# Performance work log

Hardware: AMD Instinct MI355X
Metric: run time of the kernel (lower is better)

Reference implementation:

```python
import jax, jax.numpy as jnp
import numpy as np
from jax import lax

# ---- fixed RPN/FPN configuration (torchvision defaults) ----
LEVEL_HW = [(200, 200), (100, 100), (50, 50), (25, 25), (13, 13)]
STRIDES = [4, 8, 16, 32, 64]
SIZES = [32.0, 64.0, 128.0, 256.0, 512.0]
RATIOS = [0.5, 1.0, 2.0]
A = len(RATIOS)
NUM_PER_LEVEL = [A * h * w for h, w in LEVEL_HW]
T = sum(NUM_PER_LEVEL)
N_IMG = 8
IMG_H = IMG_W = 800.0
PRE_NMS = 1000   # per level
POST_NMS = 1000
NMS_TH = 0.7
MIN_SIZE = 1e-3
BBOX_CLIP = float(np.log(1000.0 / 16.0))


def _make_anchors():
    all_a = []
    for (h, w), s, size in zip(LEVEL_HW, STRIDES, SIZES):
        base = []
        for r in RATIOS:
            bw = size / np.sqrt(r)
            bh = size * np.sqrt(r)
            base.append([-bw / 2, -bh / 2, bw / 2, bh / 2])
        base = np.asarray(base, np.float32)                      # [A,4]
        ys = (np.arange(h, dtype=np.float32) + 0.5) * s
        xs = (np.arange(w, dtype=np.float32) + 0.5) * s
        cy, cx = np.meshgrid(ys, xs, indexing='ij')
        shifts = np.stack([cx, cy, cx, cy], -1).reshape(-1, 1, 4)  # [H*W,1,4]
        all_a.append((shifts + base[None]).reshape(-1, 4))         # [H*W*A,4]
    return np.concatenate(all_a, 0)                                # [T,4]


def setup_inputs() -> dict:
    key = jax.random.key(0)
    k1, k2 = jax.random.split(key)
    objectness = jax.random.normal(k1, (N_IMG, T), jnp.float32)
    deltas = jax.random.normal(k2, (N_IMG, T, 4), jnp.float32) * 0.2
    anchors = jnp.asarray(_make_anchors())
    return {"objectness": objectness, "deltas": deltas, "anchors": anchors}


def _decode(deltas, anchors):
    # BoxCoder.decode with weights (1,1,1,1)
    w = anchors[:, 2] - anchors[:, 0]
    h = anchors[:, 3] - anchors[:, 1]
    cx = anchors[:, 0] + 0.5 * w
    cy = anchors[:, 1] + 0.5 * h
    dx, dy, dw, dh = deltas[..., 0], deltas[..., 1], deltas[..., 2], deltas[..., 3]
    dw = jnp.minimum(dw, BBOX_CLIP)
    dh = jnp.minimum(dh, BBOX_CLIP)
    pcx = dx * w + cx
    pcy = dy * h + cy
    pw = jnp.exp(dw) * w
    ph = jnp.exp(dh) * h
    return jnp.stack([pcx - 0.5 * pw, pcy - 0.5 * ph,
                      pcx + 0.5 * pw, pcy + 0.5 * ph], axis=-1)  # [N,T,4]


def _pairwise_iou(b):
    area = (b[:, 2] - b[:, 0]) * (b[:, 3] - b[:, 1])
    lt = jnp.maximum(b[:, None, :2], b[None, :, :2])
    rb = jnp.minimum(b[:, None, 2:], b[None, :, 2:])
    wh = jnp.clip(rb - lt, 0.0)
    inter = wh[..., 0] * wh[..., 1]
    return inter / (area[:, None] + area[None, :] - inter)


def _per_image(args):
    boxes, logit, lvl = args          # [K,4], [K], [K]
    # clip to image
    x1 = jnp.clip(boxes[:, 0], 0.0, IMG_W)
    y1 = jnp.clip(boxes[:, 1], 0.0, IMG_H)
    x2 = jnp.clip(boxes[:, 2], 0.0, IMG_W)
    y2 = jnp.clip(boxes[:, 3], 0.0, IMG_H)
    boxes_c = jnp.stack([x1, y1, x2, y2], -1)
    # small-box filter -> mask via -inf score
    valid = (x2 - x1 >= MIN_SIZE) & (y2 - y1 >= MIN_SIZE)
    scores = jax.nn.sigmoid(logit)
    s = jnp.where(valid, scores, -jnp.inf)
    # batched NMS: offset boxes per level so cross-level IoU == 0
    max_c = boxes_c.max()
    off = lvl.astype(boxes_c.dtype) * (max_c + 1.0)
    bn = boxes_c + off[:, None]
    order = jnp.argsort(-s)
    b = bn[order]
    sv = s[order]
    so = scores[order]
    bo = boxes_c[order]
    K = b.shape[0]
    iou = _pairwise_iou(b)
    idx = jnp.arange(K)

    def body(i, supp):
        alive = jnp.logical_not(supp[i])
        sup_i = alive & (iou[i] > NMS_TH) & (idx > i)
        return supp | sup_i

    supp = lax.fori_loop(0, K, body, jnp.zeros((K,), bool))
    keep = jnp.logical_not(supp) & jnp.isfinite(sv)
    sel_s = jnp.where(keep, sv, -jnp.inf)
    vals, sel = lax.top_k(sel_s, POST_NMS)      # post-nms top-n (sorted desc)
    vmask = jnp.isfinite(vals)
    out_boxes = jnp.where(vmask[:, None], bo[sel], 0.0)
    out_scores = jnp.where(vmask, so[sel], 0.0)
    return jnp.concatenate([out_boxes, out_scores[:, None]], -1)  # [P,5]


def reference(objectness, deltas, anchors):
    proposals = _decode(deltas, anchors)            # [N,T,4]
    # per-level top-k of objectness (get_top_n_idx)
    idxs = []
    offset = 0
    for n in NUM_PER_LEVEL:
        ob = lax.slice_in_dim(objectness, offset, offset + n, axis=1)
        k = min(PRE_NMS, n)
        _, top = lax.top_k(ob, k)
        idxs.append(top + offset)
        offset += n
    top_idx = jnp.concatenate(idxs, axis=1)         # [N,K]
    levels_full = jnp.concatenate(
        [jnp.full((n,), i, jnp.int32) for i, n in enumerate(NUM_PER_LEVEL)])
    logit_g = jnp.take_along_axis(objectness, top_idx, axis=1)          # [N,K]
    props_g = jnp.take_along_axis(proposals, top_idx[..., None], axis=1)  # [N,K,4]
    lvl_g = levels_full[top_idx]                                        # [N,K]
    out = lax.map(_per_image, (props_g, logit_g, lvl_g))                # [N,P,5]
    return out
```

## Files before the change

kernel.cpp:

```cpp
#include <hip/hip_runtime.h>
#include <math.h>

#define NIMG 8
#define TT   159882
#define KTOT 4507
#define POST 1000
#define NSUB 32

__constant__ int c_n[5]   = {120000,30000,7500,1875,507};
__constant__ int c_off[5] = {0,120000,150000,157500,159375};
__constant__ int c_k[5]   = {1000,1000,1000,1000,507};
__constant__ int c_pos[5] = {0,1000,2000,3000,4000};

__device__ __forceinline__ unsigned fkey(float f){
  unsigned u=__float_as_uint(f);
  return (u&0x80000000u)? ~u : (u|0x80000000u);
}

__global__ __launch_bounds__(256) void k_zero(unsigned* __restrict__ ghist,
                                              int* __restrict__ grank,
                                              unsigned* __restrict__ gmaxu){
  int i=blockIdx.x*256+threadIdx.x;
  if(i<40*2048) ghist[i]=0u;
  int j=i-40*2048;
  if(j>=0 && j<NIMG*KTOT) grank[j]=0;
  int j2=j-NIMG*KTOT;
  if(j2>=0 && j2<NIMG) gmaxu[j2]=0u;
}

template<int RND>
__global__ __launch_bounds__(256) void k_hist(const float* __restrict__ obj,
    const unsigned* __restrict__ gpref, unsigned* __restrict__ ghist){
  constexpr int sh=(RND==0)?21:10;
  constexpr unsigned msk=2047u;
  const int il=blockIdx.x, sub=blockIdx.y;
  const int img=il/5, lvl=il%5;
  const int n=c_n[lvl], k=c_k[lvl];
  if(k>=n) return;
  const int chunk=(n+NSUB-1)/NSUB;
  const int start=sub*chunk, end=min(start+chunk,n);
  if(start>=end) return;
  const float* o=obj+(size_t)img*TT+c_off[lvl];
  __shared__ unsigned hist[2048];
  const unsigned prefix=(RND==0)?0u:gpref[il];
  for(int i=threadIdx.x;i<2048;i+=256) hist[i]=0u;
  __syncthreads();
  for(int i=start+threadIdx.x;i<end;i+=256){
    unsigned key=fkey(o[i]);
    if(RND==0){
      atomicAdd(&hist[(key>>sh)&msk],1u);
    } else {
      if((key&0xFFE00000u)==prefix) atomicAdd(&hist[(key>>sh)&msk],1u);
    }
  }
  __syncthreads();
  for(int b=threadIdx.x;b<2048;b+=256){
    unsigned v=hist[b];
    if(v) atomicAdd(&ghist[il*2048+b],v);
  }
}

template<int RND>
__global__ __launch_bounds__(256) void k_scan(unsigned* __restrict__ ghist,
    unsigned* __restrict__ gpref, int* __restrict__ gkrem,
    int* __restrict__ gcnt){
  constexpr int sh=(RND==0)?21:10;
  constexpr int C=8;
  const int il=blockIdx.x, lvl=il%5;
  const int n=c_n[lvl], k=c_k[lvl];
  const int t=threadIdx.x;
  __shared__ unsigned tot[256];
  if(k>=n){
    if(RND==1 && t==0){ gpref[il]=0u; gkrem[il]=0; gcnt[il*2]=0; gcnt[il*2+1]=0; }
    return;
  }
  const int kr=(RND==0)?k:gkrem[il];
  unsigned v[C];
#pragma unroll
  for(int i=0;i<C;i++) v[i]=ghist[il*2048+t*C+i];
#pragma unroll
  for(int i=C-2;i>=0;i--) v[i]+=v[i+1];
  tot[t]=v[0];
  __syncthreads();
#pragma unroll
  for(int d=1;d<256;d<<=1){
    unsigned add=(t+d<256)?tot[t+d]:0u;
    __syncthreads();
    tot[t]+=add;
    __syncthreads();
  }
  unsigned tail=(t<255)?tot[t+1]:0u;
#pragma unroll
  for(int i=0;i<C;i++){
    unsigned suf=v[i]+tail;
    unsigned sufn=((i<C-1)?v[i+1]:0u)+tail;
    if(suf>=(unsigned)kr && sufn<(unsigned)kr){
      unsigned prevPref=(RND==0)?0u:gpref[il];
      gpref[il]=prevPref|((unsigned)(t*C+i)<<sh);
      gkrem[il]=kr-(int)sufn;
    }
  }
  for(int b=t;b<2048;b+=256) ghist[il*2048+b]=0u;
  if(RND==1 && t==0){ gcnt[il*2]=0; gcnt[il*2+1]=0; }
}

__global__ __launch_bounds__(256) void k_sel(const float* __restrict__ obj,
    const unsigned* __restrict__ gpref, const int* __restrict__ gkrem,
    int* __restrict__ gcnt, int* __restrict__ sel, int* __restrict__ eqbuf){
  const int il=blockIdx.x, sub=blockIdx.y;
  const int img=il/5, lvl=il%5;
  const int n=c_n[lvl], k=c_k[lvl];
  const int chunk=(n+NSUB-1)/NSUB;
  const int start=sub*chunk, end=min(start+chunk,n);
  if(start>=end) return;
  int* s=sel+img*KTOT+c_pos[lvl];
  if(k>=n){
    for(int i=start+threadIdx.x;i<end;i+=256) s[i]=i;
    return;
  }
  __shared__ int s_gt[1024];
  __shared__ int s_eq[2048];
  __shared__ int cnt_gt, cnt_eq, base_gt, base_eq;
  if(threadIdx.x==0){ cnt_gt=0; cnt_eq=0; }
  __syncthreads();
  const float* o=obj+(size_t)img*TT+c_off[lvl];
  const unsigned t=gpref[il];
  const int krem=gkrem[il];
  for(int i=start+threadIdx.x;i<end;i+=256){
    unsigned mk=fkey(o[i])&0xFFFFFC00u;
    if(mk>t){ int p=atomicAdd(&cnt_gt,1); s_gt[p]=i; }
    else if(mk==t && krem>0){ int p=atomicAdd(&cnt_eq,1); if(p<2048) s_eq[p]=i; }
  }
  __syncthreads();
  const int cg=cnt_gt, ce=min(cnt_eq,2048);
  if(threadIdx.x==0) base_gt=(cg>0)? atomicAdd(&gcnt[il*2],cg) : 0;
  if(threadIdx.x==1) base_eq=(ce>0)? atomicAdd(&gcnt[il*2+1],ce) : 0;
  __syncthreads();
  for(int i=threadIdx.x;i<cg;i+=256) s[base_gt+i]=s_gt[i];
  for(int i=threadIdx.x;i<ce;i+=256){
    int p=base_eq+i;
    if(p<2048) eqbuf[il*2048+p]=s_eq[i];
  }
}

__global__ __launch_bounds__(256) void k_sortd(const float* __restrict__ obj,
    const int* __restrict__ gkrem, const int* __restrict__ gcnt,
    const int* __restrict__ sel, int* __restrict__ sel2,
    const int* __restrict__ eqbuf){
  const int il=blockIdx.x, chunk=blockIdx.y;
  const int img=il/5, lvl=il%5;
  const int n=c_n[lvl], k=c_k[lvl];
  if(chunk*256>=k) return;
  const float* o=obj+(size_t)img*TT+c_off[lvl];
  const int* s=sel+img*KTOT+c_pos[lvl];
  int* s2=sel2+img*KTOT+c_pos[lvl];
  __shared__ unsigned long long skey[1024];
  __shared__ unsigned long long eqk[2048];
  int cgt, krem;
  if(k<n){ cgt=gcnt[il*2]; krem=gkrem[il]; } else { cgt=k; krem=0; }
  const int ceq = (krem>0)? min(gcnt[il*2+1],2048) : 0;
  for(int i=threadIdx.x;i<cgt;i+=256){
    int idx=s[i];
    skey[i]=((unsigned long long)fkey(o[idx])<<32)|(unsigned)(~(unsigned)idx);
  }
  for(int i=threadIdx.x;i<ceq;i+=256){
    int idx=eqbuf[il*2048+i];
    eqk[i]=((unsigned long long)fkey(o[idx])<<32)|(unsigned)(~(unsigned)idx);
  }
  __syncthreads();
  if(krem>0 && threadIdx.x==0){
    for(int r2=0;r2<krem;r2++){
      unsigned long long best=0ull; int bi=0;
      for(int j=0;j<ceq;j++){ unsigned long long kk=eqk[j]; if(kk>best){best=kk;bi=j;} }
      skey[cgt+r2]=best; eqk[bi]=0ull;
    }
  }
  __syncthreads();
  const int i=chunk*256+threadIdx.x;
  if(i>=k) return;
  const unsigned long long mk=skey[i];
  int rank=0, j=0;
  const int k8=k&~7;
  for(;j<k8;j+=8){
    unsigned long long a0=skey[j  ],a1=skey[j+1],a2=skey[j+2],a3=skey[j+3];
    unsigned long long a4=skey[j+4],a5=skey[j+5],a6=skey[j+6],a7=skey[j+7];
    rank+=((a0>mk)?1:0)+((a1>mk)?1:0)+((a2>mk)?1:0)+((a3>mk)?1:0)
         +((a4>mk)?1:0)+((a5>mk)?1:0)+((a6>mk)?1:0)+((a7>mk)?1:0);
  }
  for(;j<k;j++) rank+=(skey[j]>mk)?1:0;
  int idx=(int)(~(unsigned)(mk&0xFFFFFFFFu));
  s2[rank]=idx+c_off[lvl];
}

__global__ __launch_bounds__(256) void k_decode(const float* __restrict__ obj,
    const float* __restrict__ del, const float* __restrict__ anc,
    const int* __restrict__ sel, float* __restrict__ pbox, float* __restrict__ pscore,
    int* __restrict__ plvl, unsigned long long* __restrict__ gkey,
    unsigned* __restrict__ gmaxu){
  const int img=blockIdx.x/18, chunk=blockIdx.x%18;
  const int pos=chunk*256+threadIdx.x;
  __shared__ float smax[256];
  const float BCLIP=(float)4.135166556742356;
  float lm=0.f;
  if(pos<KTOT){
    int lvl = pos<1000?0:pos<2000?1:pos<3000?2:pos<4000?3:4;
    int tdx = sel[img*KTOT+pos];
    float logit = obj[(size_t)img*TT+tdx];
    const float* a=anc+4*(size_t)tdx;
    const float* d=del+((size_t)img*TT+tdx)*4;
    float w=a[2]-a[0], h=a[3]-a[1];
    float cx=a[0]+0.5f*w, cy=a[1]+0.5f*h;
    float dw=fminf(d[2],BCLIP), dh=fminf(d[3],BCLIP);
    float pcx=d[0]*w+cx, pcy=d[1]*h+cy;
    float pw=expf(dw)*w, ph=expf(dh)*h;
    float x1=pcx-0.5f*pw, y1=pcy-0.5f*ph;
    float x2=pcx+0.5f*pw, y2=pcy+0.5f*ph;
    x1=fminf(fmaxf(x1,0.f),800.f); y1=fminf(fmaxf(y1,0.f),800.f);
    x2=fminf(fmaxf(x2,0.f),800.f); y2=fminf(fmaxf(y2,0.f),800.f);
    int valid=(x2-x1>=1e-3f)&&(y2-y1>=1e-3f);
    float sc=1.f/(1.f+expf(-logit));
    float sv=valid? sc : -INFINITY;
    gkey[img*KTOT+pos]=((unsigned long long)fkey(sv)<<32)|(unsigned)(KTOT-1-pos);
    float* pb=pbox+((size_t)img*KTOT+pos)*4;
    pb[0]=x1; pb[1]=y1; pb[2]=x2; pb[3]=y2;
    pscore[img*KTOT+pos]=sc;
    plvl[img*KTOT+pos]=lvl|(valid?0:256);
    lm=fmaxf(fmaxf(x1,y1),fmaxf(x2,y2));
  }
  smax[threadIdx.x]=lm; __syncthreads();
  for(int st=128;st>0;st>>=1){
    if(threadIdx.x<st) smax[threadIdx.x]=fmaxf(smax[threadIdx.x],smax[threadIdx.x+st]);
    __syncthreads();
  }
  if(threadIdx.x==0) atomicMax(&gmaxu[img], __float_as_uint(smax[0]));
}

__global__ __launch_bounds__(256) void k_rankp(const unsigned long long* __restrict__ gkey,
    int* __restrict__ grank){
  const int img=blockIdx.x, ic=blockIdx.y, jc=blockIdx.z;
  __shared__ unsigned long long sk[256];
  const int jbase=jc*256;
  const int jend=min(256, KTOT-jbase);
  const int i=ic*256+threadIdx.x;
  if(threadIdx.x<jend) sk[threadIdx.x]=gkey[img*KTOT+jbase+threadIdx.x];
  __syncthreads();
  if(i>=KTOT) return;
  const unsigned long long mk=gkey[img*KTOT+i];
  int r=0;
  #pragma unroll 4
  for(int j=0;j<jend;j++) r+=(sk[j]>mk)?1:0;
  if(r) atomicAdd(&grank[img*KTOT+i], r);
}

__global__ __launch_bounds__(256) void k_scatter(const int* __restrict__ grank,
    const float4* __restrict__ pbox, const float* __restrict__ pscore,
    const int* __restrict__ plvl,
    float4* __restrict__ sbox, float* __restrict__ sscore,
    int* __restrict__ slvl, int* __restrict__ ssupp){
  const int img=blockIdx.x/18, chunk=blockIdx.x%18;
  const int pos=chunk*256+threadIdx.x;
  if(pos>=KTOT) return;
  const int rank=grank[img*KTOT+pos];
  sbox[(size_t)img*KTOT+rank]=pbox[(size_t)img*KTOT+pos];
  sscore[img*KTOT+rank]=pscore[img*KTOT+pos];
  int lv=plvl[img*KTOT+pos];
  slvl[img*KTOT+rank]=lv&0xFF;
  ssupp[img*KTOT+rank]=(lv>>8)&1;
}

__global__ __launch_bounds__(256) void k_list(const float* __restrict__ sbox,
    const int* __restrict__ slvl, const int* __restrict__ ssupp,
    const unsigned* __restrict__ gmaxu,
    int* __restrict__ lists, int* __restrict__ mcnt,
    float4* __restrict__ nbox, float* __restrict__ narea){
  const int img=blockIdx.x/5, lvl=blockIdx.x%5;
  const int tid=threadIdx.x;
  __shared__ unsigned char s_ok[KTOT];
  __shared__ int s_list[1024];
  __shared__ int s_m;
  for(int i=tid;i<KTOT;i+=256)
    s_ok[i]=(slvl[img*KTOT+i]==lvl && ssupp[img*KTOT+i]==0)?1:0;
  __syncthreads();
  if(tid<64){
    int base=0;
    for(int t=0;t<KTOT;t+=64){
      int r=t+tid;
      bool pred=(r<KTOT) && s_ok[r];
      unsigned long long b=__ballot(pred);
      int pre=__popcll(b & ((1ull<<tid)-1ull));
      if(pred) s_list[base+pre]=r;
      base+=__popcll(b);
    }
    if(tid==0){ s_m=base; mcnt[blockIdx.x]=base; }
  }
  __syncthreads();
  const int m=s_m;
  const float off=(float)lvl*(__uint_as_float(gmaxu[img])+1.0f);
  const float4* sb4=(const float4*)sbox;
  for(int i=tid;i<m;i+=256){
    int r=s_list[i];
    lists[blockIdx.x*1024+i]=r;
    float4 bx=sb4[(size_t)img*KTOT+r];
    float a0=bx.x+off, a1=bx.y+off, a2=bx.z+off, a3=bx.w+off;
    nbox[blockIdx.x*1024+i]=make_float4(a0,a1,a2,a3);
    narea[blockIdx.x*1024+i]=(a2-a0)*(a3-a1);
  }
}

__global__ __launch_bounds__(256) void k_mask(const float4* __restrict__ nbox,
    const float* __restrict__ narea, const int* __restrict__ mcnt,
    unsigned long long* __restrict__ mask){
  const int il=blockIdx.x;
  const int rc=blockIdx.y>>4, w=blockIdx.y&15;
  const int m=mcnt[il];
  const int r0=rc*256;
  if(r0>=m) return;
  const int i=r0+threadIdx.x;
  const int wlast=(m+63)>>6;
  __shared__ float4 sb[64];
  __shared__ float  sa[64];
  unsigned long long bits=0ull;
  const bool block_active = (w>=rc*4) && (w<wlast);
  if(block_active){
    const int jend=min(64, m-w*64);
    if(threadIdx.x<64 && threadIdx.x<jend){
      sb[threadIdx.x]=nbox[il*1024+w*64+threadIdx.x];
      sa[threadIdx.x]=narea[il*1024+w*64+threadIdx.x];
    }
    __syncthreads();
    const int wi=i>>6;
    if(i<m && w>=wi){
      const float4 bi=nbox[il*1024+i];
      const float  ai=narea[il*1024+i];
      for(int jj=0;jj<jend;++jj){
        const float4 bj=sb[jj];
        float ltx=fmaxf(bi.x,bj.x), lty=fmaxf(bi.y,bj.y);
        float rbx=fminf(bi.z,bj.z), rby=fminf(bi.w,bj.w);
        float wx=fmaxf(rbx-ltx,0.f), wy=fmaxf(rby-lty,0.f);
        float inter=wx*wy;
        float iou=inter/((ai+sa[jj])-inter);
        bits |= (iou>0.7f)? (1ull<<jj) : 0ull;
      }
      if(w==wi){ int b=i&63; bits &= ~((2ull<<b)-1ull); }
    }
  }
  if(i<m) mask[((size_t)il*1024+i)*16+w]=bits;
}

__global__ __launch_bounds__(256) void k_reduce(const unsigned long long* __restrict__ mask,
    const int* __restrict__ mcnt, const int* __restrict__ lists,
    int* __restrict__ ssupp){
  const int il=blockIdx.x, img=il/5;
  const int m=mcnt[il];
  const int m_pad=(m+15)&~15;
  __shared__ unsigned long long smask[1024*16];
  {
    const float4* g4=(const float4*)(mask + (size_t)il*1024*16);
    float4* l4=(float4*)smask;
    const int tot4=(m*8+2047)&~2047;
    for(int i=threadIdx.x;i<tot4;i+=2048){
      float4 r0=g4[i      ], r1=g4[i+ 256], r2=g4[i+ 512], r3=g4[i+ 768];
      float4 r4=g4[i+1024], r5=g4[i+1280], r6=g4[i+1536], r7=g4[i+1792];
      l4[i      ]=r0; l4[i+ 256]=r1; l4[i+ 512]=r2; l4[i+ 768]=r3;
      l4[i+1024]=r4; l4[i+1280]=r5; l4[i+1536]=r6; l4[i+1792]=r7;
    }
  }
  __syncthreads();
  if(threadIdx.x<(m_pad-m)*16) smask[(unsigned)m*16+threadIdx.x]=0ull;
  __syncthreads();
  if(threadIdx.x>=64) return;
  const int lane=threadIdx.x;
  const int seg=lane&15;
  unsigned long long remv=0ull;
  unsigned long long c0,c1,c2,c3,c4,c5,c6,c7,c8,c9,c10,c11,c12,c13,c14,c15;
  unsigned long long n0,n1,n2,n3,n4,n5,n6,n7,n8,n9,n10,n11,n12,n13,n14,n15;
#define LD(r,b) smask[(unsigned)((b)+(r))*16+seg]
  c0 =LD(0,0);  c1 =LD(1,0);  c2 =LD(2,0);  c3 =LD(3,0);
  c4 =LD(4,0);  c5 =LD(5,0);  c6 =LD(6,0);  c7 =LD(7,0);
  c8 =LD(8,0);  c9 =LD(9,0);  c10=LD(10,0); c11=LD(11,0);
  c12=LD(12,0); c13=LD(13,0); c14=LD(14,0); c15=LD(15,0);
  for(int g=0;;++g){
    const int nb=(g+1)*16;
    n0 =LD(0,nb);  n1 =LD(1,nb);  n2 =LD(2,nb);  n3 =LD(3,nb);
    n4 =LD(4,nb);  n5 =LD(5,nb);  n6 =LD(6,nb);  n7 =LD(7,nb);
    n8 =LD(8,nb);  n9 =LD(9,nb);  n10=LD(10,nb); n11=LD(11,nb);
    n12=LD(12,nb); n13=LD(13,nb); n14=LD(14,nb); n15=LD(15,nb);
    const int base=g*16;
    const int w=base>>6;
    const int bb=base&63;
    unsigned t8=(unsigned)(remv>>bb);
    unsigned am=0u;
#define DEC(r,cr) { unsigned alive=1u^((t8>>(r))&1u); am|=alive<<(r); \
                    if(alive) t8|=(unsigned)((cr)>>bb); }
    DEC(0,c0)  DEC(1,c1)  DEC(2,c2)  DEC(3,c3)
    DEC(4,c4)  DEC(5,c5)  DEC(6,c6)  DEC(7,c7)
    DEC(8,c8)  DEC(9,c9)  DEC(10,c10) DEC(11,c11)
    DEC(12,c12) DEC(13,c13) DEC(14,c14) DEC(15,c15)
#undef DEC
    unsigned am_w=__builtin_amdgcn_readlane(am, w);
#define APP(r,cr) { unsigned long long mk64=0ull-(unsigned long long)((am_w>>(r))&1u); \
                    remv|=(cr)&mk64; }
    APP(0,c0)  APP(1,c1)  APP(2,c2)  APP(3,c3)
    APP(4,c4)  APP(5,c5)  APP(6,c6)  APP(7,c7)
    APP(8,c8)  APP(9,c9)  APP(10,c10) APP(11,c11)
    APP(12,c12) APP(13,c13) APP(14,c14) APP(15,c15)
#undef APP
    if(nb>=m) break;
    c0 =n0;  c1 =n1;  c2 =n2;  c3 =n3;  c4 =n4;  c5 =n5;  c6 =n6;  c7 =n7;
    c8 =n8;  c9 =n9;  c10=n10; c11=n11; c12=n12; c13=n13; c14=n14; c15=n15;
  }
#undef LD
  const int* list = lists + il*1024;
  for(int t=0;t<m;t+=64){
    int i=t+lane;
    unsigned long long word=__shfl(remv, (i<m? i:0)>>6);
    if(i<m && ((word>>(i&63))&1ull)) ssupp[img*KTOT+list[i]]=1;
  }
}

__global__ __launch_bounds__(256) void k_out(const float* __restrict__ sbox,
    const float* __restrict__ sscore, const int* __restrict__ ssupp,
    float* __restrict__ out){
  const int img=blockIdx.x;
  const int tid=threadIdx.x;
  __shared__ unsigned char s_ok[KTOT];
  __shared__ unsigned short list[POST];
  __shared__ int s_c;
  for(int i=tid;i<KTOT;i+=256) s_ok[i]=(ssupp[img*KTOT+i]==0)?1:0;
  __syncthreads();
  if(tid<64){
    int base=0;
    for(int t=0;t<KTOT && base<POST;t+=64){
      int r=t+tid;
      bool pred=(r<KTOT) && s_ok[r];
      unsigned long long b=__ballot(pred);
      int pre=__popcll(b & ((1ull<<tid)-1ull));
      if(pred && base+pre<POST) list[base+pre]=(unsigned short)r;
      base+=__popcll(b);
    }
    if(tid==0) s_c=min(base,POST);
  }
  __syncthreads();
  const int c=s_c;
  for(int o=tid;o<POST;o+=256){
    float* row=out+((size_t)img*POST+o)*5;
    if(o<c){
      int r=list[o];
      const float* b=sbox+((size_t)img*KTOT+r)*4;
      row[0]=b[0]; row[1]=b[1]; row[2]=b[2]; row[3]=b[3];
      row[4]=sscore[img*KTOT+r];
    } else {
      row[0]=0.f; row[1]=0.f; row[2]=0.f; row[3]=0.f; row[4]=0.f;
    }
  }
}

extern "C" void kernel_launch(void* const* d_in, const int* in_sizes, int n_in,
                              void* d_out, int out_size, void* d_ws, size_t ws_size,
                              hipStream_t stream){
  const float* obj=(const float*)d_in[0];
  const float* del=(const float*)d_in[1];
  const float* anc=(const float*)d_in[2];
  float* out=(float*)d_out;

  char* w=(char*)d_ws;
  size_t off=0;
  auto alloc=[&](size_t bytes)->void*{
    void* p=w+off; off+=(bytes+255)&~(size_t)255; return p;
  };
  int*  sel    =(int*)  alloc(sizeof(int)*NIMG*KTOT);
  int*  sel2   =(int*)  alloc(sizeof(int)*NIMG*KTOT);
  float* pbox  =(float*)alloc(sizeof(float)*NIMG*KTOT*4);
  float* pscore=(float*)alloc(sizeof(float)*NIMG*KTOT);
  int*  plvl   =(int*)  alloc(sizeof(int)*NIMG*KTOT);
  unsigned long long* gkey=(unsigned long long*)alloc(sizeof(unsigned long long)*NIMG*KTOT);
  float* sbox  =(float*)alloc(sizeof(float)*NIMG*KTOT*4);
  float* sscore=(float*)alloc(sizeof(float)*NIMG*KTOT);
  int*  slvl   =(int*)  alloc(sizeof(int)*NIMG*KTOT);
  int*  ssupp  =(int*)  alloc(sizeof(int)*NIMG*KTOT);
  unsigned* gmaxu=(unsigned*)alloc(sizeof(unsigned)*NIMG);
  int*  eqbuf  =(int*)  alloc(sizeof(int)*40*2048);
  int*  lists  =(int*)  alloc(sizeof(int)*40*1024);
  int*  mcnt   =(int*)  alloc(sizeof(int)*40);
  float4* nbox =(float4*)alloc(sizeof(float4)*40*1024);
  float* narea =(float*)alloc(sizeof(float)*40*1024);
  unsigned long long* mask=(unsigned long long*)alloc(sizeof(unsigned long long)*40*1024*16);
  unsigned* ghist=(unsigned*)alloc(sizeof(unsigned)*40*2048);
  unsigned* gpref=(unsigned*)alloc(sizeof(unsigned)*40);
  int*  gkrem  =(int*)  alloc(sizeof(int)*40);
  int*  gcnt   =(int*)  alloc(sizeof(int)*80);
  int*  grank  =(int*)  alloc(sizeof(int)*NIMG*KTOT);

  hipLaunchKernelGGL(k_zero,    dim3((40*2048+NIMG*KTOT+NIMG+255)/256), dim3(256), 0, stream,
                     ghist, grank, gmaxu);
  hipLaunchKernelGGL(k_hist<0>, dim3(40,NSUB), dim3(256), 0, stream, obj, gpref, ghist);
  hipLaunchKernelGGL(k_scan<0>, dim3(40), dim3(256), 0, stream, ghist, gpref, gkrem, gcnt);
  hipLaunchKernelGGL(k_hist<1>, dim3(40,NSUB), dim3(256), 0, stream, obj, gpref, ghist);
  hipLaunchKernelGGL(k_scan<1>, dim3(40), dim3(256), 0, stream, ghist, gpref, gkrem, gcnt);
  hipLaunchKernelGGL(k_sel,    dim3(40,NSUB), dim3(256), 0, stream, obj, gpref, gkrem,
                     gcnt, sel, eqbuf);
  hipLaunchKernelGGL(k_sortd,  dim3(40,4), dim3(256), 0, stream, obj, gkrem, gcnt,
                     sel, sel2, eqbuf);
  hipLaunchKernelGGL(k_decode, dim3(NIMG*18), dim3(256), 0, stream, obj, del, anc, sel2,
                     pbox, pscore, plvl, gkey, gmaxu);
  hipLaunchKernelGGL(k_rankp,  dim3(NIMG,18,18), dim3(256), 0, stream, gkey, grank);
  hipLaunchKernelGGL(k_scatter,dim3(NIMG*18), dim3(256), 0, stream, grank,
                     (const float4*)pbox, pscore, plvl,
                     (float4*)sbox, sscore, slvl, ssupp);
  hipLaunchKernelGGL(k_list,   dim3(40), dim3(256), 0, stream, sbox, slvl, ssupp, gmaxu,
                     lists, mcnt, nbox, narea);
  hipLaunchKernelGGL(k_mask,   dim3(40,64), dim3(256), 0, stream, nbox, narea, mcnt, mask);
  hipLaunchKernelGGL(k_reduce, dim3(40), dim3(256), 0, stream, mask, mcnt, lists, ssupp);
  hipLaunchKernelGGL(k_out,    dim3(NIMG), dim3(256), 0, stream, sbox, sscore, ssupp, out);
}
```

Baseline: 152.1 us.

## Replace two-pass radix top-k select with single pass plus parallel tie ranking

Result: slower. 392.1 us (+157.8%).

```diff
diff --git a/kernel.cpp b/kernel.cpp
--- a/kernel.cpp
+++ b/kernel.cpp
@@ -18,21 +18,15 @@
 }
 
 __global__ __launch_bounds__(256) void k_zero(unsigned* __restrict__ ghist,
-                                              int* __restrict__ grank,
-                                              unsigned* __restrict__ gmaxu){
+                                              int* __restrict__ grank){
   int i=blockIdx.x*256+threadIdx.x;
   if(i<40*2048) ghist[i]=0u;
   int j=i-40*2048;
   if(j>=0 && j<NIMG*KTOT) grank[j]=0;
-  int j2=j-NIMG*KTOT;
-  if(j2>=0 && j2<NIMG) gmaxu[j2]=0u;
-}
-
-template<int RND>
+}
+
 __global__ __launch_bounds__(256) void k_hist(const float* __restrict__ obj,
-    const unsigned* __restrict__ gpref, unsigned* __restrict__ ghist){
-  constexpr int sh=(RND==0)?21:10;
-  constexpr unsigned msk=2047u;
+    unsigned* __restrict__ ghist){
   const int il=blockIdx.x, sub=blockIdx.y;
   const int img=il/5, lvl=il%5;
   const int n=c_n[lvl], k=c_k[lvl];
@@ -42,16 +36,11 @@
   if(start>=end) return;
   const float* o=obj+(size_t)img*TT+c_off[lvl];
   __shared__ unsigned hist[2048];
-  const unsigned prefix=(RND==0)?0u:gpref[il];
   for(int i=threadIdx.x;i<2048;i+=256) hist[i]=0u;
   __syncthreads();
   for(int i=start+threadIdx.x;i<end;i+=256){
     unsigned key=fkey(o[i]);
-    if(RND==0){
-      atomicAdd(&hist[(key>>sh)&msk],1u);
-    } else {
-      if((key&0xFFE00000u)==prefix) atomicAdd(&hist[(key>>sh)&msk],1u);
-    }
+    atomicAdd(&hist[key>>21],1u);
   }
   __syncthreads();
   for(int b=threadIdx.x;b<2048;b+=256){
@@ -60,21 +49,21 @@
   }
 }
 
-template<int RND>
 __global__ __launch_bounds__(256) void k_scan(unsigned* __restrict__ ghist,
     unsigned* __restrict__ gpref, int* __restrict__ gkrem,
-    int* __restrict__ gcnt){
-  constexpr int sh=(RND==0)?21:10;
+    int* __restrict__ gcnt, unsigned* __restrict__ gmaxu){
   constexpr int C=8;
   const int il=blockIdx.x, lvl=il%5;
   const int n=c_n[lvl], k=c_k[lvl];
   const int t=threadIdx.x;
   __shared__ unsigned tot[256];
+  if(t==0 && il<NIMG) gmaxu[il]=0u;
+  if(t==0){ gcnt[il*2]=0; gcnt[il*2+1]=0; }
   if(k>=n){
-    if(RND==1 && t==0){ gpref[il]=0u; gkrem[il]=0; gcnt[il*2]=0; gcnt[il*2+1]=0; }
+    if(t==0){ gpref[il]=0u; gkrem[il]=0; }
     return;
   }
-  const int kr=(RND==0)?k:gkrem[il];
+  const int kr=k;
   unsigned v[C];
 #pragma unroll
   for(int i=0;i<C;i++) v[i]=ghist[il*2048+t*C+i];
@@ -95,13 +84,11 @@
     unsigned suf=v[i]+tail;
     unsigned sufn=((i<C-1)?v[i+1]:0u)+tail;
     if(suf>=(unsigned)kr && sufn<(unsigned)kr){
-      unsigned prevPref=(RND==0)?0u:gpref[il];
-      gpref[il]=prevPref|((unsigned)(t*C+i)<<sh);
+      gpref[il]=(unsigned)(t*C+i)<<21;
       gkrem[il]=kr-(int)sufn;
     }
   }
   for(int b=t;b<2048;b+=256) ghist[il*2048+b]=0u;
-  if(RND==1 && t==0){ gcnt[il*2]=0; gcnt[il*2+1]=0; }
 }
 
 __global__ __launch_bounds__(256) void k_sel(const float* __restrict__ obj,
@@ -127,7 +114,7 @@
   const unsigned t=gpref[il];
   const int krem=gkrem[il];
   for(int i=start+threadIdx.x;i<end;i+=256){
-    unsigned mk=fkey(o[i])&0xFFFFFC00u;
+    unsigned mk=fkey(o[i])&0xFFE00000u;
     if(mk>t){ int p=atomicAdd(&cnt_gt,1); s_gt[p]=i; }
     else if(mk==t && krem>0){ int p=atomicAdd(&cnt_eq,1); if(p<2048) s_eq[p]=i; }
   }
@@ -139,7 +126,7 @@
   for(int i=threadIdx.x;i<cg;i+=256) s[base_gt+i]=s_gt[i];
   for(int i=threadIdx.x;i<ce;i+=256){
     int p=base_eq+i;
-    if(p<2048) eqbuf[il*2048+p]=s_eq[i];
+    if(p<4096) eqbuf[il*4096+p]=s_eq[i];
   }
 }
 
@@ -155,25 +142,24 @@
   const int* s=sel+img*KTOT+c_pos[lvl];
   int* s2=sel2+img*KTOT+c_pos[lvl];
   __shared__ unsigned long long skey[1024];
-  __shared__ unsigned long long eqk[2048];
+  __shared__ unsigned long long eqk[4096];
   int cgt, krem;
   if(k<n){ cgt=gcnt[il*2]; krem=gkrem[il]; } else { cgt=k; krem=0; }
-  const int ceq = (krem>0)? min(gcnt[il*2+1],2048) : 0;
+  const int ceq = (krem>0)? min(gcnt[il*2+1],4096) : 0;
   for(int i=threadIdx.x;i<cgt;i+=256){
     int idx=s[i];
     skey[i]=((unsigned long long)fkey(o[idx])<<32)|(unsigned)(~(unsigned)idx);
   }
   for(int i=threadIdx.x;i<ceq;i+=256){
-    int idx=eqbuf[il*2048+i];
+    int idx=eqbuf[il*4096+i];
     eqk[i]=((unsigned long long)fkey(o[idx])<<32)|(unsigned)(~(unsigned)idx);
   }
   __syncthreads();
-  if(krem>0 && threadIdx.x==0){
-    for(int r2=0;r2<krem;r2++){
-      unsigned long long best=0ull; int bi=0;
-      for(int j=0;j<ceq;j++){ unsigned long long kk=eqk[j]; if(kk>best){best=kk;bi=j;} }
-      skey[cgt+r2]=best; eqk[bi]=0ull;
-    }
+  for(int i=threadIdx.x;i<ceq;i+=256){
+    unsigned long long mk=eqk[i];
+    int r=0;
+    for(int j=0;j<ceq;j++) r+=(eqk[j]>mk)?1:0;
+    if(r<krem) skey[cgt+r]=mk;
   }
   __syncthreads();
   const int i=chunk*256+threadIdx.x;
@@ -479,7 +465,7 @@
   int*  slvl   =(int*)  alloc(sizeof(int)*NIMG*KTOT);
   int*  ssupp  =(int*)  alloc(sizeof(int)*NIMG*KTOT);
   unsigned* gmaxu=(unsigned*)alloc(sizeof(unsigned)*NIMG);
-  int*  eqbuf  =(int*)  alloc(sizeof(int)*40*2048);
+  int*  eqbuf  =(int*)  alloc(sizeof(int)*40*4096);
   int*  lists  =(int*)  alloc(sizeof(int)*40*1024);
   int*  mcnt   =(int*)  alloc(sizeof(int)*40);
   float4* nbox =(float4*)alloc(sizeof(float4)*40*1024);
@@ -491,25 +477,24 @@
   int*  gcnt   =(int*)  alloc(sizeof(int)*80);
   int*  grank  =(int*)  alloc(sizeof(int)*NIMG*KTOT);
 
-  hipLaunchKernelGGL(k_zero,    dim3((40*2048+NIMG*KTOT+NIMG+255)/256), dim3(256), 0, stream,
-                     ghist, grank, gmaxu);
-  hipLaunchKernelGGL(k_hist<0>, dim3(40,NSUB), dim3(256), 0, stream, obj, gpref, ghist);
-  hipLaunchKernelGGL(k_scan<0>, dim3(40), dim3(256), 0, stream, ghist, gpref, gkrem, gcnt);
-  hipLaunchKernelGGL(k_hist<1>, dim3(40,NSUB), dim3(256), 0, stream, obj, gpref, ghist);
-  hipLaunchKernelGGL(k_scan<1>, dim3(40), dim3(256), 0, stream, ghist, gpref, gkrem, gcnt);
-  hipLaunchKernelGGL(k_sel,    dim3(40,NSUB), dim3(256), 0, stream, obj, gpref, gkrem,
+  hipLaunchKernelGGL(k_zero,    dim3((40*2048+NIMG*KTOT+255)/256), dim3(256), 0, stream,
+                     ghist, grank);
+  hipLaunchKernelGGL(k_hist,    dim3(40,NSUB), dim3(256), 0, stream, obj, ghist);
+  hipLaunchKernelGGL(k_scan,    dim3(40), dim3(256), 0, stream, ghist, gpref, gkrem,
+                     gcnt, gmaxu);
+  hipLaunchKernelGGL(k_sel,     dim3(40,NSUB), dim3(256), 0, stream, obj, gpref, gkrem,
                      gcnt, sel, eqbuf);
-  hipLaunchKernelGGL(k_sortd,  dim3(40,4), dim3(256), 0, stream, obj, gkrem, gcnt,
+  hipLaunchKernelGGL(k_sortd,   dim3(40,4), dim3(256), 0, stream, obj, gkrem, gcnt,
                      sel, sel2, eqbuf);
-  hipLaunchKernelGGL(k_decode, dim3(NIMG*18), dim3(256), 0, stream, obj, del, anc, sel2,
+  hipLaunchKernelGGL(k_decode,  dim3(NIMG*18), dim3(256), 0, stream, obj, del, anc, sel2,
                      pbox, pscore, plvl, gkey, gmaxu);
-  hipLaunchKernelGGL(k_rankp,  dim3(NIMG,18,18), dim3(256), 0, stream, gkey, grank);
-  hipLaunchKernelGGL(k_scatter,dim3(NIMG*18), dim3(256), 0, stream, grank,
+  hipLaunchKernelGGL(k_rankp,   dim3(NIMG,18,18), dim3(256), 0, stream, gkey, grank);
+  hipLaunchKernelGGL(k_scatter, dim3(NIMG*18), dim3(256), 0, stream, grank,
                      (const float4*)pbox, pscore, plvl,
                      (float4*)sbox, sscore, slvl, ssupp);
-  hipLaunchKernelGGL(k_list,   dim3(40), dim3(256), 0, stream, sbox, slvl, ssupp, gmaxu,
+  hipLaunchKernelGGL(k_list,    dim3(40), dim3(256), 0, stream, sbox, slvl, ssupp, gmaxu,
                      lists, mcnt, nbox, narea);
-  hipLaunchKernelGGL(k_mask,   dim3(40,64), dim3(256), 0, stream, nbox, narea, mcnt, mask);
-  hipLaunchKernelGGL(k_reduce, dim3(40), dim3(256), 0, stream, mask, mcnt, lists, ssupp);
-  hipLaunchKernelGGL(k_out,    dim3(NIMG), dim3(256), 0, stream, sbox, sscore, ssupp, out);
-}
+  hipLaunchKernelGGL(k_mask,    dim3(40,64), dim3(256), 0, stream, nbox, narea, mcnt, mask);
+  hipLaunchKernelGGL(k_reduce,  dim3(40), dim3(256), 0, stream, mask, mcnt, lists, ssupp);
+  hipLaunchKernelGGL(k_out,     dim3(NIMG), dim3(256), 0, stream, sbox, sscore, ssupp, out);
+}
```
